# Kernel tuning notes

Measured on AMD Instinct MI355X. Metric: run time of the kernel, lower is better.

## Reference

```python
import math
import jax, jax.numpy as jnp
import numpy as np

B, S, DIM = 1, 1024, 2048
H, KVH, HD = 16, 4, 128
HID, L, VOCAB = 8192, 2, 32000
NIMG, TOK_START = 256, 1
IMG_IN = 2 * 14 * 14 * 3  # temporal_patch*spatial_patch^2*channels
EPS = 1e-6


def _rms(x, w=None, eps=EPS):
    y = x * jax.lax.rsqrt(jnp.mean(x * x, axis=-1, keepdims=True) + eps)
    return y if w is None else y * w


def _rope(x, angles):
    # x: [B,S,H,D], angles: [S, D//2] pairwise rotation angles (3D RoPE: 1D+2D concat)
    c = jnp.cos(angles)[None, :, None, :]
    s = jnp.sin(angles)[None, :, None, :]
    x1, x2 = x[..., 0::2], x[..., 1::2]
    return jnp.stack([x1 * c - x2 * s, x1 * s + x2 * c], axis=-1).reshape(x.shape)


def setup_inputs() -> dict:
    key = jax.random.key(0)
    ks = jax.random.split(key, 12)
    sc = 0.02
    return {
        "tokens": jax.random.randint(ks[0], (B, S), 0, VOCAB),
        "img_feats": jax.random.normal(ks[1], (B, NIMG, IMG_IN), jnp.float32),
        "freqs_cis": jax.random.normal(ks[2], (S, HD // 4), jnp.float32),
        "freqs_cis_2d": jax.random.normal(ks[3], (S, HD // 4), jnp.float32),
        "tok_emb": jax.random.normal(ks[4], (VOCAB, DIM), jnp.float32) * sc,
        "img_proj_w": jax.random.normal(ks[5], (DIM, IMG_IN), jnp.float32) * sc,
        "wqkv": jax.random.normal(ks[6], (L, H * HD + 2 * KVH * HD, DIM), jnp.float32) * sc,
        "wo": jax.random.normal(ks[7], (L, DIM, H * HD), jnp.float32) * sc,
        "sinks": jax.random.normal(ks[8], (L, H), jnp.float32),
        "w13": jax.random.normal(ks[9], (L, 2 * HID, DIM), jnp.float32) * sc,
        "w2": jax.random.normal(ks[10], (L, DIM, HID), jnp.float32) * sc,
        "norm_w": jnp.ones((DIM,), jnp.float32),
        "output_w": jax.random.normal(ks[11], (VOCAB, DIM), jnp.float32) * sc,
    }


def reference(tokens, img_feats, freqs_cis, freqs_cis_2d, tok_emb, img_proj_w,
              wqkv, wo, sinks, w13, w2, norm_w, output_w):
    # token embeddings + slice-based scatter of projected image tokens
    x = tok_emb[tokens]                                   # [B,S,DIM]
    img = jnp.einsum('bnf,df->bnd', img_feats, img_proj_w)
    x = jax.lax.dynamic_update_slice(x, img, (0, TOK_START, 0))

    angles = jnp.concatenate([freqs_cis, freqs_cis_2d], axis=-1)  # [S, HD//2]
    scale = 1.0 / math.sqrt(HD)
    neg = jnp.where(jnp.tril(jnp.ones((S, S), bool)), 0.0, -jnp.inf)  # causal
    n_rep = H // KVH
    q_dim, kv_dim = H * HD, KVH * HD

    for i in range(L):
        # attention: RMSNorm -> QKV -> QK-norm -> GQA expand -> RoPE -> SDPA+lse
        h = _rms(x)
        qkv = h @ wqkv[i].T
        q = qkv[..., :q_dim].reshape(B, S, H, HD)
        k = qkv[..., q_dim:q_dim + kv_dim].reshape(B, S, KVH, HD)
        v = qkv[..., q_dim + kv_dim:].reshape(B, S, KVH, HD)
        q, k = _rms(q), _rms(k)
        k = jnp.repeat(k, n_rep, axis=2)  # repeat_interleave over kv heads
        v = jnp.repeat(v, n_rep, axis=2)
        q, k = _rope(q, angles), _rope(k, angles)
        scores = jnp.einsum('bqhd,bkhd->bhqk', q, k) * scale + neg
        lse = jax.nn.logsumexp(scores, axis=-1)            # [B,H,S]
        attn = jnp.exp(scores - lse[..., None])
        out = jnp.einsum('bhqk,bkhd->bqhd', attn, v)        # [B,S,H,HD]
        sink_scale = jax.nn.sigmoid(lse - sinks[i][None, :, None])  # [B,H,S]
        out = out * sink_scale.transpose(0, 2, 1)[..., None]
        x = x + out.reshape(B, S, H * HD) @ wo[i].T

        # FFN: RMSNorm -> interleaved gate/up -> relu(gate)^2 * up -> down
        h = _rms(x)
        packed = h @ w13[i].T
        gate, up = packed[..., 0::2], packed[..., 1::2]
        x = x + (jnp.square(jax.nn.relu(gate)) * up) @ w2[i].T

    return _rms(x, norm_w) @ output_w.T                    # [B,S,VOCAB]
```

## Files before the change

kernel.cpp:

```cpp
#include <hip/hip_runtime.h>

typedef __bf16 bf16;
typedef bf16 bf16x8 __attribute__((ext_vector_type(8)));
typedef bf16 bf16x4 __attribute__((ext_vector_type(4)));
typedef bf16 bf16x2 __attribute__((ext_vector_type(2)));
typedef float f32x4 __attribute__((ext_vector_type(4)));
typedef float f32x2 __attribute__((ext_vector_type(2)));

#define S_LEN 1024
#define DIM 2048
#define NH 16
#define NKVH 4
#define HD 128
#define HID 8192
#define VOCAB 32000
#define QKV_N 3072
#define W13_N 16384
#define IMG_K 1176
#define NIMG 256

#define AS1 __attribute__((address_space(1)))
#define AS3 __attribute__((address_space(3)))

__device__ inline f32x4 mfma16(bf16x8 a, bf16x8 b, f32x4 c) {
  return __builtin_amdgcn_mfma_f32_16x16x32_bf16(a, b, c, 0, 0, 0);
}

__global__ void embed_kernel(const int* __restrict__ tok, const float* __restrict__ emb,
                             float* __restrict__ x) {
  int s = blockIdx.x, t = threadIdx.x;
  int id = tok[s];
  const float* er = emb + (size_t)id * DIM;
  float* xr = x + (size_t)s * DIM;
  *(f32x4*)(xr + t * 8)     = *(const f32x4*)(er + t * 8);
  *(f32x4*)(xr + t * 8 + 4) = *(const f32x4*)(er + t * 8 + 4);
}

__global__ void cvt_kernel(const float* __restrict__ in, bf16* __restrict__ o, int n) {
  int i = blockIdx.x * 256 + threadIdx.x;
  if (i < n) o[i] = (bf16)in[i];
}
__global__ void cvt4_kernel(const float* __restrict__ in, bf16* __restrict__ o, int n4) {
  int i = blockIdx.x * 256 + threadIdx.x;
  if (i < n4) {
    f32x4 v = *(const f32x4*)(in + (size_t)i * 4);
    bf16x4 b;
    b[0] = (bf16)v[0]; b[1] = (bf16)v[1]; b[2] = (bf16)v[2]; b[3] = (bf16)v[3];
    *(bf16x4*)(o + (size_t)i * 4) = b;
  }
}

template<int USE_W>
__global__ void rmsnorm_kernel(const float* __restrict__ x, const float* __restrict__ w,
                               bf16* __restrict__ o) {
  const int row = blockIdx.x, t = threadIdx.x;
  const float* xr = x + (size_t)row * DIM;
  f32x4 a = *(const f32x4*)(xr + t * 8);
  f32x4 b = *(const f32x4*)(xr + t * 8 + 4);
  float ss = a[0]*a[0] + a[1]*a[1] + a[2]*a[2] + a[3]*a[3]
           + b[0]*b[0] + b[1]*b[1] + b[2]*b[2] + b[3]*b[3];
#pragma unroll
  for (int off = 1; off < 64; off <<= 1) ss += __shfl_xor(ss, off);
  __shared__ float red[4];
  if ((t & 63) == 0) red[t >> 6] = ss;
  __syncthreads();
  ss = red[0] + red[1] + red[2] + red[3];
  float r = rsqrtf(ss * (1.0f / DIM) + 1e-6f);
  bf16x8 ov;
  if (USE_W) {
    f32x4 w1 = *(const f32x4*)(w + t * 8);
    f32x4 w2v = *(const f32x4*)(w + t * 8 + 4);
    ov[0] = (bf16)(a[0]*r*w1[0]); ov[1] = (bf16)(a[1]*r*w1[1]);
    ov[2] = (bf16)(a[2]*r*w1[2]); ov[3] = (bf16)(a[3]*r*w1[3]);
    ov[4] = (bf16)(b[0]*r*w2v[0]); ov[5] = (bf16)(b[1]*r*w2v[1]);
    ov[6] = (bf16)(b[2]*r*w2v[2]); ov[7] = (bf16)(b[3]*r*w2v[3]);
  } else {
    ov[0] = (bf16)(a[0]*r); ov[1] = (bf16)(a[1]*r);
    ov[2] = (bf16)(a[2]*r); ov[3] = (bf16)(a[3]*r);
    ov[4] = (bf16)(b[0]*r); ov[5] = (bf16)(b[1]*r);
    ov[6] = (bf16)(b[2]*r); ov[7] = (bf16)(b[3]*r);
  }
  *(bf16x8*)(o + (size_t)row * DIM + t * 8) = ov;
}

__global__ void qkvpost_kernel(const float* __restrict__ qkv, const float* __restrict__ f1,
                               const float* __restrict__ f2, bf16* __restrict__ qb,
                               bf16* __restrict__ kb, bf16* __restrict__ vtb) {
  int s = blockIdx.x, t = threadIdx.x;
  __shared__ float cs[64], sn[64];
  if (t < 64) {
    float ang = (t < 32) ? f1[(size_t)s * 32 + t] : f2[(size_t)s * 32 + (t - 32)];
    cs[t] = cosf(ang);
    sn[t] = sinf(ang);
  }
  __syncthreads();
  int w = t >> 6, lane = t & 63;
  for (int hh = w; hh < 24; hh += 4) {
    const float* base = qkv + (size_t)s * QKV_N + hh * HD;
    f32x2 e = *(const f32x2*)(base + lane * 2);
    if (hh < 20) {
      float ssum = e[0]*e[0] + e[1]*e[1];
#pragma unroll
      for (int off = 1; off < 64; off <<= 1) ssum += __shfl_xor(ssum, off);
      float r = rsqrtf(ssum * (1.0f / HD) + 1e-6f);
      float x1 = e[0] * r, x2 = e[1] * r;
      float c = cs[lane], s2 = sn[lane];
      bf16x2 ov;
      ov[0] = (bf16)(x1 * c - x2 * s2);
      ov[1] = (bf16)(x1 * s2 + x2 * c);
      if (hh < 16)
        *(bf16x2*)(qb + ((size_t)hh * S_LEN + s) * HD + lane * 2) = ov;
      else
        *(bf16x2*)(kb + ((size_t)(hh - 16) * S_LEN + s) * HD + lane * 2) = ov;
    } else {
      int kv = hh - 20;
      vtb[((size_t)kv * HD + lane * 2) * S_LEN + s]     = (bf16)e[0];
      vtb[((size_t)kv * HD + lane * 2 + 1) * S_LEN + s] = (bf16)e[1];
    }
  }
}

__global__ void attn_kernel(const bf16* __restrict__ qb, const bf16* __restrict__ kb,
                            const bf16* __restrict__ vtb, const float* __restrict__ sinks,
                            bf16* __restrict__ out) {
  const int h = blockIdx.y, qblk = blockIdx.x;
  const int w = threadIdx.x >> 6, lane = threadIdx.x & 63;
  const int lo = lane & 15, hi = lane >> 4;
  const int q0 = qblk * 64 + w * 16;
  const int q = q0 + lo;
  const int kvh = h >> 2;
  const bf16* Q = qb + (size_t)h * S_LEN * HD;
  const bf16* Kp = kb + (size_t)kvh * S_LEN * HD;
  const bf16* Vt = vtb + (size_t)kvh * HD * S_LEN;
  const float scale = 0.08838834764831845f;

  bf16x8 qf[4];
#pragma unroll
  for (int ks = 0; ks < 4; ++ks)
    qf[ks] = *(const bf16x8*)(Q + (size_t)q * HD + ks * 32 + hi * 8);

  f32x4 accT[8];
#pragma unroll
  for (int i = 0; i < 8; ++i) accT[i] = (f32x4){0.f, 0.f, 0.f, 0.f};
  float mrow = -3e38f, lrow = 0.f;

  const int nt = (q0 + 15) / 32 + 1;
  for (int tile = 0; tile < nt; ++tile) {
    const int kv0 = tile * 32;
    f32x4 st0 = (f32x4){0.f,0.f,0.f,0.f}, st1 = (f32x4){0.f,0.f,0.f,0.f};
#pragma unroll
    for (int ks = 0; ks < 4; ++ks) {
      const bf16* kbase = Kp + (size_t)(kv0 + lo) * HD + ks * 32 + hi * 8;
      bf16x8 k0f = *(const bf16x8*)(kbase);
      bf16x8 k1f = *(const bf16x8*)(kbase + 16 * HD);
      st0 = mfma16(k0f, qf[ks], st0);
      st1 = mfma16(k1f, qf[ks], st1);
    }
    float p[2][4];
    float pmax = -3e38f;
#pragma unroll
    for (int r = 0; r < 4; ++r) {
      int kvg0 = kv0 + hi * 4 + r;
      float v0 = (kvg0 <= q) ? st0[r] * scale : -3e38f;
      int kvg1 = kvg0 + 16;
      float v1 = (kvg1 <= q) ? st1[r] * scale : -3e38f;
      p[0][r] = v0; p[1][r] = v1;
      pmax = fmaxf(pmax, fmaxf(v0, v1));
    }
    pmax = fmaxf(pmax, __shfl_xor(pmax, 16));
    pmax = fmaxf(pmax, __shfl_xor(pmax, 32));
    float mnew = fmaxf(mrow, pmax);
    float alpha = __expf(mrow - mnew);
    float ps = 0.f;
#pragma unroll
    for (int f = 0; f < 2; ++f)
#pragma unroll
      for (int r = 0; r < 4; ++r) {
        float e = __expf(p[f][r] - mnew);
        p[f][r] = e;
        ps += e;
      }
    ps += __shfl_xor(ps, 16);
    ps += __shfl_xor(ps, 32);
    lrow = lrow * alpha + ps;
    mrow = mnew;
#pragma unroll
    for (int fd = 0; fd < 8; ++fd) {
      accT[fd][0] *= alpha; accT[fd][1] *= alpha;
      accT[fd][2] *= alpha; accT[fd][3] *= alpha;
    }
    bf16x8 pb;
#pragma unroll
    for (int j = 0; j < 8; ++j) {
      int src = ((j >> 2) + 2 * (hi & 1)) * 16 + lo;
      float v0 = __shfl(p[0][j & 3], src);
      float v1 = __shfl(p[1][j & 3], src);
      pb[j] = (bf16)((hi >= 2) ? v1 : v0);
    }
#pragma unroll
    for (int fd = 0; fd < 8; ++fd) {
      bf16x8 vf = *(const bf16x8*)(Vt + (size_t)(fd * 16 + lo) * S_LEN + kv0 + hi * 8);
      accT[fd] = mfma16(vf, pb, accT[fd]);
    }
  }
  float lse = mrow + __logf(lrow);
  float ssig = 1.f / (1.f + __expf(sinks[h] - lse));
  float sc = ssig / lrow;
#pragma unroll
  for (int fd = 0; fd < 8; ++fd)
#pragma unroll
    for (int r = 0; r < 4; ++r)
      out[(size_t)q * DIM + h * HD + fd * 16 + hi * 4 + r] = (bf16)(accT[fd][r] * sc);
}

__device__ inline void xcd_remap(int ntm, int ntn, int& mtile, int& ntile) {
  const int flat = blockIdx.x + ntm * blockIdx.y;
  const int chunk = ntm * 8;
  const int gfull = ntn >> 3;
  const int g = flat / chunk;
  if (g < gfull) {
    int rem = flat - g * chunk;
    ntile = g * 8 + (rem & 7);
    mtile = rem >> 3;
  } else {
    int rem = flat - gfull * chunk;
    int nrem = ntn - gfull * 8;
    ntile = gfull * 8 + rem % nrem;
    mtile = rem / nrem;
  }
}

enum { EPI_STORE = 0, EPI_ADD = 1, EPI_ACT = 2 };

template<int BM, int BN, int EPI, int GL>
__global__ void gemm_bt(const bf16* __restrict__ A, const float* __restrict__ W,
                        float* __restrict__ C, bf16* __restrict__ Cb,
                        int M, int N, int K, int ldc) {
  constexpr int BK = 64;
  __shared__ __align__(16) char lds[(BM + BN) * BK * 2];
  char* ldsA = lds;
  char* ldsB = lds + BM * BK * 2;
  const int t = threadIdx.x;
  int mtile, ntile;
  xcd_remap(gridDim.x, gridDim.y, mtile, ntile);
  const int m0 = mtile * BM, n0 = ntile * BN;

  const int wid = t >> 6, lane = t & 63;
  const int lo = lane & 15, hi = lane >> 4;
  const int wr = wid >> 1, wc = wid & 1;
  constexpr int TM = BM / 32, TN = BN / 32;
  constexpr int NA = BM / 32;
  constexpr int NPASS = BM / 32;
  constexpr int NW = BN / 16;

  f32x4 acc[TM][TN];
#pragma unroll
  for (int m = 0; m < TM; ++m)
#pragma unroll
    for (int n = 0; n < TN; ++n) acc[m][n] = (f32x4){0.f, 0.f, 0.f, 0.f};

  const int nk = (K + BK - 1) / BK;
  for (int kt = 0; kt < nk; ++kt) {
    const int k0 = kt * BK;
    bf16x8 av[NA];
    f32x4 wv[NW];
    if (!GL) {
#pragma unroll
      for (int i = 0; i < NA; ++i) {
        int c = t + i * 256;
        int row = c >> 3, kc = c & 7;
        int kg = k0 + kc * 8;
        bf16x8 z = {};
        av[i] = (kg < K) ? *(const bf16x8*)(A + (size_t)(m0 + row) * K + kg) : z;
      }
    }
#pragma unroll
    for (int i = 0; i < NW; ++i) {
      int c = t + i * 256;
      int row = c >> 4, kc = c & 15;
      int kg = k0 + kc * 4;
      f32x4 z = (f32x4){0.f, 0.f, 0.f, 0.f};
      wv[i] = (kg < K) ? *(const f32x4*)(W + (size_t)(n0 + row) * K + kg) : z;
    }
    __syncthreads();
    if (GL) {
#pragma unroll
      for (int i = 0; i < NPASS; ++i) {
        int row = i * 32 + (t >> 3);
        int srcb = ((t & 7) * 16) ^ ((row & 7) << 4);
        const bf16* g2 = A + (size_t)(m0 + row) * K + k0 + (srcb >> 1);
        char* l = ldsA + i * 4096 + wid * 1024;
        __builtin_amdgcn_global_load_lds((const AS1 void*)g2, (AS3 void*)l, 16, 0, 0);
      }
    } else {
#pragma unroll
      for (int i = 0; i < NA; ++i) {
        int c = t + i * 256;
        int row = c >> 3, kc = c & 7;
        int kb = (kc * 16) ^ ((row & 7) << 4);
        *(bf16x8*)(ldsA + row * 128 + kb) = av[i];
      }
    }
#pragma unroll
    for (int i = 0; i < NW; ++i) {
      int c = t + i * 256;
      int row = c >> 4, kc = c & 15;
      bf16x4 bv;
      bv[0] = (bf16)wv[i][0]; bv[1] = (bf16)wv[i][1];
      bv[2] = (bf16)wv[i][2]; bv[3] = (bf16)wv[i][3];
      int kb = (kc * 8) ^ ((row & 7) << 4);
      *(bf16x4*)(ldsB + row * 128 + kb) = bv;
    }
    __syncthreads();
#pragma unroll
    for (int ks = 0; ks < 2; ++ks) {
      bf16x8 af[TM], bfr[TN];
      int kbb = ks * 64 + hi * 16;
#pragma unroll
      for (int m = 0; m < TM; ++m) {
        int row = wr * (BM / 2) + m * 16 + lo;
        af[m] = *(const bf16x8*)(ldsA + row * 128 + (kbb ^ ((row & 7) << 4)));
      }
#pragma unroll
      for (int n = 0; n < TN; ++n) {
        int row = wc * (BN / 2) + n * 16 + lo;
        bfr[n] = *(const bf16x8*)(ldsB + row * 128 + (kbb ^ ((row & 7) << 4)));
      }
#pragma unroll
      for (int m = 0; m < TM; ++m)
#pragma unroll
        for (int n = 0; n < TN; ++n)
          acc[m][n] = mfma16(af[m], bfr[n], acc[m][n]);
    }
    __syncthreads();
  }
#pragma unroll
  for (int m = 0; m < TM; ++m) {
    int gmb = m0 + wr * (BM / 2) + m * 16 + hi * 4;
#pragma unroll
    for (int n = 0; n < TN; ++n) {
      int gn = n0 + wc * (BN / 2) + n * 16 + lo;
#pragma unroll
      for (int r = 0; r < 4; ++r) {
        float v = acc[m][n][r];
        if (EPI == EPI_STORE) {
          C[(size_t)(gmb + r) * ldc + gn] = v;
        } else if (EPI == EPI_ADD) {
          C[(size_t)(gmb + r) * ldc + gn] += v;
        } else {
          float pv = __shfl_xor(v, 1);
          if (!(lane & 1)) {
            float g2 = fmaxf(v, 0.f);
            Cb[(size_t)(gmb + r) * (W13_N / 2) + (gn >> 1)] = (bf16)(g2 * g2 * pv);
          }
        }
      }
    }
  }
}

template<int BM, int BN, int EPI>
__global__ __launch_bounds__(256) void gemm_bb(const bf16* __restrict__ A,
                                               const bf16* __restrict__ W,
                                               float* __restrict__ C, bf16* __restrict__ Cb,
                                               int K, int ldc) {
  constexpr int BK = 64;
  __shared__ __align__(16) char lds[(BM + BN) * BK * 2];
  char* ldsA = lds;
  char* ldsB = lds + BM * BK * 2;
  const int t = threadIdx.x;
  int mtile, ntile;
  xcd_remap(gridDim.x, gridDim.y, mtile, ntile);
  const int m0 = mtile * BM, n0 = ntile * BN;

  const int wid = t >> 6, lane = t & 63;
  const int lo = lane & 15, hi = lane >> 4;
  const int wr = wid >> 1, wc = wid & 1;
  constexpr int TM = BM / 32, TN = BN / 32;
  constexpr int PA = BM / 32, PB = BN / 32;

  f32x4 acc[TM][TN];
#pragma unroll
  for (int m = 0; m < TM; ++m)
#pragma unroll
    for (int n = 0; n < TN; ++n) acc[m][n] = (f32x4){0.f, 0.f, 0.f, 0.f};

  const int prow = t >> 3;
  const int psrcb = (t & 7) * 16;
  const int nk = K / BK;
  for (int kt = 0; kt < nk; ++kt) {
    const int k0 = kt * BK;
#pragma unroll
    for (int i = 0; i < PA; ++i) {
      int row = i * 32 + prow;
      int srcb = psrcb ^ ((row & 7) << 4);
      const bf16* g = A + (size_t)(m0 + row) * K + k0 + (srcb >> 1);
      __builtin_amdgcn_global_load_lds((const AS1 void*)g,
                                       (AS3 void*)(ldsA + i * 4096 + wid * 1024), 16, 0, 0);
    }
#pragma unroll
    for (int i = 0; i < PB; ++i) {
      int row = i * 32 + prow;
      int srcb = psrcb ^ ((row & 7) << 4);
      const bf16* g = W + (size_t)(n0 + row) * K + k0 + (srcb >> 1);
      __builtin_amdgcn_global_load_lds((const AS1 void*)g,
                                       (AS3 void*)(ldsB + i * 4096 + wid * 1024), 16, 0, 0);
    }
    __syncthreads();
#pragma unroll
    for (int ks = 0; ks < 2; ++ks) {
      bf16x8 af[TM], bfr[TN];
      int kbb = ks * 64 + hi * 16;
#pragma unroll
      for (int m = 0; m < TM; ++m) {
        int row = wr * (BM / 2) + m * 16 + lo;
        af[m] = *(const bf16x8*)(ldsA + row * 128 + (kbb ^ ((row & 7) << 4)));
      }
#pragma unroll
      for (int n = 0; n < TN; ++n) {
        int row = wc * (BN / 2) + n * 16 + lo;
        bfr[n] = *(const bf16x8*)(ldsB + row * 128 + (kbb ^ ((row & 7) << 4)));
      }
#pragma unroll
      for (int m = 0; m < TM; ++m)
#pragma unroll
        for (int n = 0; n < TN; ++n)
          acc[m][n] = mfma16(af[m], bfr[n], acc[m][n]);
    }
    __syncthreads();
  }
#pragma unroll
  for (int m = 0; m < TM; ++m) {
    int gmb = m0 + wr * (BM / 2) + m * 16 + hi * 4;
#pragma unroll
    for (int n = 0; n < TN; ++n) {
      int gn = n0 + wc * (BN / 2) + n * 16 + lo;
#pragma unroll
      for (int r = 0; r < 4; ++r) {
        float v = acc[m][n][r];
        if (EPI == EPI_STORE) {
          C[(size_t)(gmb + r) * ldc + gn] = v;
        } else if (EPI == EPI_ADD) {
          C[(size_t)(gmb + r) * ldc + gn] += v;
        } else {
          float pv = __shfl_xor(v, 1);
          if (!(lane & 1)) {
            float g2 = fmaxf(v, 0.f);
            Cb[(size_t)(gmb + r) * (W13_N / 2) + (gn >> 1)] = (bf16)(g2 * g2 * pv);
          }
        }
      }
    }
  }
}

template<int EPI>
__global__ __launch_bounds__(512, 1) void gemm_2pf(const bf16* __restrict__ A,
                                                   const float* __restrict__ W,
                                                   float* __restrict__ C, bf16* __restrict__ Cb,
                                                   int K, int ldc) {
  extern __shared__ __align__(16) char lds[];
  char* ldsA = lds;
  char* ldsB = lds + 65536;
  const int t = threadIdx.x;
  int mtile, ntile;
  xcd_remap(gridDim.x, gridDim.y, mtile, ntile);
  const int m0 = mtile * 256, n0 = ntile * 256;
  const int wid = t >> 6, lane = t & 63;
  const int lo = lane & 15, hi = lane >> 4;
  const int wr = wid >> 2, wc = wid & 3;

  f32x4 acc[8][4];
#pragma unroll
  for (int f = 0; f < 8; ++f)
#pragma unroll
    for (int g = 0; g < 4; ++g) acc[f][g] = (f32x4){0.f, 0.f, 0.f, 0.f};

  const int prow = t >> 3;
  const int pcol = (t & 7) * 16;

  auto STAGEA = [&](int h, int kt2) {
    char* dst = ldsA + (kt2 & 1) * 32768 + h * 16384;
    const int k0 = kt2 * 64;
#pragma unroll
    for (int i = 0; i < 2; ++i) {
      int row = i * 64 + prow;
      int srcb = pcol ^ ((row & 7) << 4);
      const bf16* g = A + (size_t)(m0 + h * 128 + row) * K + k0 + (srcb >> 1);
      __builtin_amdgcn_global_load_lds((const AS1 void*)g,
          (AS3 void*)(dst + i * 8192 + wid * 1024), 16, 0, 0);
    }
  };

  f32x4 breg[4][2];
  auto BLOAD = [&](int kt2) {
#pragma unroll
    for (int i = 0; i < 4; ++i) {
      int c = t + i * 512;
      int row = c >> 3, kc = c & 7;
      const float* g = W + (size_t)(n0 + row) * K + kt2 * 64 + kc * 8;
      breg[i][0] = *(const f32x4*)(g);
      breg[i][1] = *(const f32x4*)(g + 4);
    }
  };
  auto BWRITE = [&](int kt2) {
#pragma unroll
    for (int i = 0; i < 4; ++i) {
      int c = t + i * 512;
      int row = c >> 3, kc = c & 7;
      int h = row >> 7, rowh = row & 127;
      bf16x8 bv;
#pragma unroll
      for (int e = 0; e < 4; ++e) {
        bv[e]     = (bf16)breg[i][0][e];
        bv[4 + e] = (bf16)breg[i][1][e];
      }
      *(bf16x8*)(ldsB + (kt2 & 1) * 32768 + h * 16384 + rowh * 128 +
                 ((kc * 16) ^ ((rowh & 7) << 4))) = bv;
    }
  };

  auto LDA = [&](int buf, int mh, int i, int ks) -> bf16x8 {
    int row = (mh * 4 + i) * 16 + lo;
    return *(const bf16x8*)(ldsA + buf * 32768 + wr * 16384 + row * 128 +
                            ((ks * 64 + hi * 16) ^ ((row & 7) << 4)));
  };
  auto LDB = [&](int buf, int nh, int j, int ks) -> bf16x8 {
    int rowh = (wc & 1) * 64 + (nh * 2 + j) * 16 + lo;
    return *(const bf16x8*)(ldsB + buf * 32768 + (wc >> 1) * 16384 + rowh * 128 +
                            ((ks * 64 + hi * 16) ^ ((rowh & 7) << 4)));
  };

  const int nk = K / 64;
  BLOAD(0);
  STAGEA(0, 0);
  STAGEA(1, 0);
  BWRITE(0);
  asm volatile("s_waitcnt vmcnt(0) lgkmcnt(0)" ::: "memory");
  __builtin_amdgcn_s_barrier();

  for (int kt = 0; kt < nk; ++kt) {
    const int buf = kt & 1;
    const bool more = (kt + 1) < nk;
    if (more) {
      BLOAD(kt + 1);
      STAGEA(0, kt + 1);
      STAGEA(1, kt + 1);
    }
#pragma unroll
    for (int mh = 0; mh < 2; ++mh) {
      bf16x8 a[4][2];
#pragma unroll
      for (int i = 0; i < 4; ++i) { a[i][0] = LDA(buf, mh, i, 0); a[i][1] = LDA(buf, mh, i, 1); }
#pragma unroll
      for (int nh = 0; nh < 2; ++nh) {
        bf16x8 b[2][2];
#pragma unroll
        for (int j = 0; j < 2; ++j) { b[j][0] = LDB(buf, nh, j, 0); b[j][1] = LDB(buf, nh, j, 1); }
        asm volatile("s_waitcnt lgkmcnt(0)" ::: "memory");
        __builtin_amdgcn_sched_barrier(0);
        __builtin_amdgcn_s_setprio(1);
#pragma unroll
        for (int i = 0; i < 4; ++i)
#pragma unroll
          for (int j = 0; j < 2; ++j) {
            acc[mh * 4 + i][nh * 2 + j] = mfma16(a[i][0], b[j][0], acc[mh * 4 + i][nh * 2 + j]);
            acc[mh * 4 + i][nh * 2 + j] = mfma16(a[i][1], b[j][1], acc[mh * 4 + i][nh * 2 + j]);
          }
        __builtin_amdgcn_s_setprio(0);
      }
    }
    if (more) BWRITE(kt + 1);
    asm volatile("s_waitcnt vmcnt(0) lgkmcnt(0)" ::: "memory");
    __builtin_amdgcn_s_barrier();
  }
#pragma unroll
  for (int f = 0; f < 8; ++f) {
    int gmb = m0 + wr * 128 + f * 16 + hi * 4;
#pragma unroll
    for (int g = 0; g < 4; ++g) {
      int gn = n0 + wc * 64 + g * 16 + lo;
#pragma unroll
      for (int r = 0; r < 4; ++r) {
        float v = acc[f][g][r];
        if (EPI == EPI_STORE) {
          C[(size_t)(gmb + r) * ldc + gn] = v;
        } else if (EPI == EPI_ADD) {
          C[(size_t)(gmb + r) * ldc + gn] += v;
        } else {
          float pv = __shfl_xor(v, 1);
          if (!(lane & 1)) {
            float g2 = fmaxf(v, 0.f);
            Cb[(size_t)(gmb + r) * (W13_N / 2) + (gn >> 1)] = (bf16)(g2 * g2 * pv);
          }
        }
      }
    }
  }
}

extern "C" void kernel_launch(void* const* d_in, const int* in_sizes, int n_in,
                              void* d_out, int out_size, void* d_ws, size_t ws_size,
                              hipStream_t stream) {
  const int* tokens = (const int*)d_in[0];
  const float* img_feats = (const float*)d_in[1];
  const float* freqs = (const float*)d_in[2];
  const float* freqs2 = (const float*)d_in[3];
  const float* tok_emb = (const float*)d_in[4];
  const float* img_proj_w = (const float*)d_in[5];
  const float* wqkv = (const float*)d_in[6];
  const float* wo = (const float*)d_in[7];
  const float* sinks = (const float*)d_in[8];
  const float* w13 = (const float*)d_in[9];
  const float* w2 = (const float*)d_in[10];
  const float* norm_w = (const float*)d_in[11];
  const float* output_w = (const float*)d_in[12];
  float* out = (float*)d_out;

  char* ws = (char*)d_ws;
  float* x = (float*)ws;   ws += (size_t)S_LEN * DIM * 4;
  bf16* h = (bf16*)ws;     ws += (size_t)S_LEN * DIM * 2;
  float* qkv = (float*)ws; ws += (size_t)S_LEN * QKV_N * 4;
  bf16* qb = (bf16*)ws;    ws += (size_t)NH * S_LEN * HD * 2;
  bf16* kb = (bf16*)ws;    ws += (size_t)NKVH * S_LEN * HD * 2;
  bf16* vtb = (bf16*)ws;   ws += (size_t)NKVH * HD * S_LEN * 2;
  bf16* ao = (bf16*)ws;    ws += (size_t)S_LEN * DIM * 2;
  bf16* act = (bf16*)ws;   ws += (size_t)S_LEN * HID * 2;
  bf16* imgb = (bf16*)ws;  ws += (size_t)NIMG * IMG_K * 2;
  const size_t n_wqkv = (size_t)2 * QKV_N * DIM;
  const size_t n_wo   = (size_t)2 * DIM * (NH * HD);
  const size_t n_w2   = (size_t)2 * DIM * HID;
  bf16* wqkvb = (bf16*)ws; ws += n_wqkv * 2;
  bf16* wob   = (bf16*)ws; ws += n_wo * 2;
  bf16* w2b   = (bf16*)ws; ws += n_w2 * 2;
  const bool bf16_path = ((size_t)(ws - (char*)d_ws) <= ws_size);

  bool big_ok = false;
  {
    hipError_t e1 = hipFuncSetAttribute((const void*)&gemm_2pf<EPI_STORE>,
                                        hipFuncAttributeMaxDynamicSharedMemorySize, 131072);
    hipError_t e2 = hipFuncSetAttribute((const void*)&gemm_2pf<EPI_ACT>,
                                        hipFuncAttributeMaxDynamicSharedMemorySize, 131072);
    if (e1 == hipSuccess && e2 == hipSuccess) {
      hipFuncAttributes fa1{}, fa2{};
      if (hipFuncGetAttributes(&fa1, (const void*)&gemm_2pf<EPI_STORE>) == hipSuccess &&
          hipFuncGetAttributes(&fa2, (const void*)&gemm_2pf<EPI_ACT>) == hipSuccess)
        big_ok = fa1.maxDynamicSharedSizeBytes >= 131072 &&
                 fa2.maxDynamicSharedSizeBytes >= 131072;
    }
  }

  embed_kernel<<<S_LEN, 256, 0, stream>>>(tokens, tok_emb, x);
  cvt_kernel<<<(NIMG * IMG_K + 255) / 256, 256, 0, stream>>>(img_feats, imgb, NIMG * IMG_K);
  gemm_bt<128, 128, EPI_STORE, 0><<<dim3(NIMG / 128, DIM / 128), 256, 0, stream>>>(
      imgb, img_proj_w, x + DIM, nullptr, NIMG, DIM, IMG_K, DIM);

  if (bf16_path) {
    cvt4_kernel<<<(int)(n_wqkv / 4 + 255) / 256, 256, 0, stream>>>(wqkv, wqkvb, (int)(n_wqkv / 4));
    cvt4_kernel<<<(int)(n_wo / 4 + 255) / 256, 256, 0, stream>>>(wo, wob, (int)(n_wo / 4));
    cvt4_kernel<<<(int)(n_w2 / 4 + 255) / 256, 256, 0, stream>>>(w2, w2b, (int)(n_w2 / 4));
  }

  for (int i = 0; i < 2; ++i) {
    rmsnorm_kernel<0><<<S_LEN, 256, 0, stream>>>(x, nullptr, h);
    if (bf16_path) {
      gemm_bb<64, 128, EPI_STORE><<<dim3(S_LEN / 64, QKV_N / 128), 256, 0, stream>>>(
          h, wqkvb + (size_t)i * QKV_N * DIM, qkv, nullptr, DIM, QKV_N);
    } else {
      gemm_bt<64, 128, EPI_STORE, 1><<<dim3(S_LEN / 64, QKV_N / 128), 256, 0, stream>>>(
          h, wqkv + (size_t)i * QKV_N * DIM, qkv, nullptr, S_LEN, QKV_N, DIM, QKV_N);
    }
    qkvpost_kernel<<<S_LEN, 256, 0, stream>>>(qkv, freqs, freqs2, qb, kb, vtb);
    attn_kernel<<<dim3(S_LEN / 64, NH), 256, 0, stream>>>(qb, kb, vtb, sinks + i * NH, ao);
    if (bf16_path) {
      gemm_bb<64, 128, EPI_ADD><<<dim3(S_LEN / 64, DIM / 128), 256, 0, stream>>>(
          ao, wob + (size_t)i * DIM * DIM, x, nullptr, DIM, DIM);
    } else {
      gemm_bt<64, 128, EPI_ADD, 1><<<dim3(S_LEN / 64, DIM / 128), 256, 0, stream>>>(
          ao, wo + (size_t)i * DIM * DIM, x, nullptr, S_LEN, DIM, DIM, DIM);
    }
    rmsnorm_kernel<0><<<S_LEN, 256, 0, stream>>>(x, nullptr, h);
    if (big_ok) {
      gemm_2pf<EPI_ACT><<<dim3(S_LEN / 256, W13_N / 256), 512, 131072, stream>>>(
          h, w13 + (size_t)i * W13_N * DIM, nullptr, act, DIM, 0);
    } else {
      gemm_bt<128, 128, EPI_ACT, 1><<<dim3(S_LEN / 128, W13_N / 128), 256, 0, stream>>>(
          h, w13 + (size_t)i * W13_N * DIM, nullptr, act, S_LEN, W13_N, DIM, 0);
    }
    if (bf16_path) {
      gemm_bb<64, 128, EPI_ADD><<<dim3(S_LEN / 64, DIM / 128), 256, 0, stream>>>(
          act, w2b + (size_t)i * DIM * HID, x, nullptr, HID, DIM);
    } else {
      gemm_bt<64, 128, EPI_ADD, 1><<<dim3(S_LEN / 64, DIM / 128), 256, 0, stream>>>(
          act, w2 + (size_t)i * DIM * HID, x, nullptr, S_LEN, DIM, HID, DIM);
    }
  }
  rmsnorm_kernel<1><<<S_LEN, 256, 0, stream>>>(x, norm_w, h);
  if (big_ok) {
    gemm_2pf<EPI_STORE><<<dim3(S_LEN / 256, VOCAB / 256), 512, 131072, stream>>>(
        h, output_w, out, nullptr, DIM, VOCAB);
  } else {
    gemm_bt<128, 128, EPI_STORE, 1><<<dim3(S_LEN / 128, VOCAB / 128), 256, 0, stream>>>(
        h, output_w, out, nullptr, S_LEN, VOCAB, DIM, VOCAB);
  }
}
```

Measured before the change: 1.117 ms.

## Split attention KV range across waves with LDS merge of partial softmax states

Each attention block now handles 16 query rows instead of 64, and its four waves stride over KV tiles. The partial max, sum and accumulator are merged through shared memory before the sink-scaled output is written. This balances the causal workload and launches four times as many blocks, at the cost of a shared-memory reduction and a barrier. The image projection GEMM also switches to a 64-row tile to get more blocks.

```diff
diff --git a/kernel.cpp b/kernel.cpp
--- a/kernel.cpp
+++ b/kernel.cpp
@@ -120,13 +120,15 @@
   }
 }
 
-__global__ void attn_kernel(const bf16* __restrict__ qb, const bf16* __restrict__ kb,
-                            const bf16* __restrict__ vtb, const float* __restrict__ sinks,
-                            bf16* __restrict__ out) {
-  const int h = blockIdx.y, qblk = blockIdx.x;
+__global__ __launch_bounds__(256) void attn_kernel(const bf16* __restrict__ qb,
+                                                   const bf16* __restrict__ kb,
+                                                   const bf16* __restrict__ vtb,
+                                                   const float* __restrict__ sinks,
+                                                   bf16* __restrict__ out) {
+  const int h = blockIdx.y, qs = blockIdx.x;
   const int w = threadIdx.x >> 6, lane = threadIdx.x & 63;
   const int lo = lane & 15, hi = lane >> 4;
-  const int q0 = qblk * 64 + w * 16;
+  const int q0 = qs * 16;
   const int q = q0 + lo;
   const int kvh = h >> 2;
   const bf16* Q = qb + (size_t)h * S_LEN * HD;
@@ -134,6 +136,9 @@
   const bf16* Vt = vtb + (size_t)kvh * HD * S_LEN;
   const float scale = 0.08838834764831845f;
 
+  __shared__ float accS[4][64 * 36];
+  __shared__ float mS[4][16], lS[4][16];
+
   bf16x8 qf[4];
 #pragma unroll
   for (int ks = 0; ks < 4; ++ks)
@@ -145,7 +150,7 @@
   float mrow = -3e38f, lrow = 0.f;
 
   const int nt = (q0 + 15) / 32 + 1;
-  for (int tile = 0; tile < nt; ++tile) {
+  for (int tile = w; tile < nt; tile += 4) {
     const int kv0 = tile * 32;
     f32x4 st0 = (f32x4){0.f,0.f,0.f,0.f}, st1 = (f32x4){0.f,0.f,0.f,0.f};
 #pragma unroll
@@ -203,14 +208,32 @@
       accT[fd] = mfma16(vf, pb, accT[fd]);
     }
   }
-  float lse = mrow + __logf(lrow);
+  if (hi == 0) { mS[w][lo] = mrow; lS[w][lo] = lrow; }
+  float* as = &accS[w][lane * 36];
+#pragma unroll
+  for (int fd = 0; fd < 8; ++fd) *(f32x4*)(as + fd * 4) = accT[fd];
+  __syncthreads();
+  float m0 = mS[0][lo], m1 = mS[1][lo], m2 = mS[2][lo], m3 = mS[3][lo];
+  float mstar = fmaxf(fmaxf(m0, m1), fmaxf(m2, m3));
+  float e0 = __expf(m0 - mstar), e1 = __expf(m1 - mstar);
+  float e2 = __expf(m2 - mstar), e3 = __expf(m3 - mstar);
+  float lstar = lS[0][lo]*e0 + lS[1][lo]*e1 + lS[2][lo]*e2 + lS[3][lo]*e3;
+  float lse = mstar + __logf(lstar);
   float ssig = 1.f / (1.f + __expf(sinks[h] - lse));
-  float sc = ssig / lrow;
-#pragma unroll
-  for (int fd = 0; fd < 8; ++fd)
-#pragma unroll
-    for (int r = 0; r < 4; ++r)
-      out[(size_t)q * DIM + h * HD + fd * 16 + hi * 4 + r] = (bf16)(accT[fd][r] * sc);
+  float sc = ssig / lstar;
+#pragma unroll
+  for (int f2 = 0; f2 < 2; ++f2) {
+    int fd = w * 2 + f2;
+    f32x4 a0 = *(const f32x4*)&accS[0][lane * 36 + fd * 4];
+    f32x4 a1 = *(const f32x4*)&accS[1][lane * 36 + fd * 4];
+    f32x4 a2 = *(const f32x4*)&accS[2][lane * 36 + fd * 4];
+    f32x4 a3 = *(const f32x4*)&accS[3][lane * 36 + fd * 4];
+#pragma unroll
+    for (int r = 0; r < 4; ++r) {
+      float o = a0[r]*e0 + a1[r]*e1 + a2[r]*e2 + a3[r]*e3;
+      out[(size_t)q * DIM + h * HD + fd * 16 + hi * 4 + r] = (bf16)(o * sc);
+    }
+  }
 }
 
 __device__ inline void xcd_remap(int ntm, int ntn, int& mtile, int& ntile) {
@@ -652,7 +675,7 @@
 
   embed_kernel<<<S_LEN, 256, 0, stream>>>(tokens, tok_emb, x);
   cvt_kernel<<<(NIMG * IMG_K + 255) / 256, 256, 0, stream>>>(img_feats, imgb, NIMG * IMG_K);
-  gemm_bt<128, 128, EPI_STORE, 0><<<dim3(NIMG / 128, DIM / 128), 256, 0, stream>>>(
+  gemm_bt<64, 128, EPI_STORE, 0><<<dim3(NIMG / 64, DIM / 128), 256, 0, stream>>>(
       imgb, img_proj_w, x + DIM, nullptr, NIMG, DIM, IMG_K, DIM);
 
   if (bf16_path) {
@@ -671,7 +694,7 @@
           h, wqkv + (size_t)i * QKV_N * DIM, qkv, nullptr, S_LEN, QKV_N, DIM, QKV_N);
     }
     qkvpost_kernel<<<S_LEN, 256, 0, stream>>>(qkv, freqs, freqs2, qb, kb, vtb);
-    attn_kernel<<<dim3(S_LEN / 64, NH), 256, 0, stream>>>(qb, kb, vtb, sinks + i * NH, ao);
+    attn_kernel<<<dim3(S_LEN / 16, NH), 256, 0, stream>>>(qb, kb, vtb, sinks + i * NH, ao);
     if (bf16_path) {
       gemm_bb<64, 128, EPI_ADD><<<dim3(S_LEN / 64, DIM / 128), 256, 0, stream>>>(
           ao, wob + (size_t)i * DIM * DIM, x, nullptr, DIM, DIM);
```

Result: faster. 1.049 ms (-6.1%).
